# Kernel tuning notes

Hardware: AMD Instinct MI355X
Metric: run time of the kernel (lower is better)

## Reference

```python
import jax, jax.numpy as jnp
import numpy as np

B, N, S = 8, 8192, 2048
D1, D2 = 128, 256
IN_CH = D1 + D2  # 384
MLP = [256, 128]
BN_EPS = 1e-5


def setup_inputs() -> dict:
    key = jax.random.key(0)
    ks = jax.random.split(key, 12)
    inp = {
        'xyz1': jax.random.normal(ks[0], (B, 3, N), dtype=jnp.float32),
        'xyz2': jax.random.normal(ks[1], (B, 3, S), dtype=jnp.float32),
        'points1': jax.random.normal(ks[2], (B, D1, N), dtype=jnp.float32),
        'points2': jax.random.normal(ks[3], (B, D2, S), dtype=jnp.float32),
    }
    # Conv1d(kernel=1) weights [out, in] + bias, BN gamma/beta per layer
    c_in = IN_CH
    for i, c_out in enumerate(MLP):
        scale = 1.0 / np.sqrt(c_in)
        inp[f'w{i}'] = jax.random.uniform(ks[4 + 2 * i], (c_out, c_in), jnp.float32, -scale, scale)
        inp[f'b{i}'] = jax.random.uniform(ks[5 + 2 * i], (c_out,), jnp.float32, -scale, scale)
        inp[f'g{i}'] = jnp.ones((c_out,), jnp.float32)
        inp[f'be{i}'] = jnp.zeros((c_out,), jnp.float32)
        c_in = c_out
    return inp


def _fp_forward(xyz1, xyz2, points1, points2, params):
    # xyz1: [B,3,N] -> [B,N,3]; xyz2: [B,3,S] -> [B,S,3]
    p1 = jnp.transpose(xyz1, (0, 2, 1))
    p2 = jnp.transpose(xyz2, (0, 2, 1))
    # squared pairwise distances [B,N,S]
    dist = (jnp.sum(p1 * p1, -1)[:, :, None]
            + jnp.sum(p2 * p2, -1)[:, None, :]
            - 2.0 * jnp.einsum('bnc,bsc->bns', p1, p2))
    # 3 smallest distances per query point
    neg_d, idx = jax.lax.top_k(-dist, 3)          # idx: [B,N,3]
    d3 = -neg_d
    recip = 1.0 / (d3 + 1e-8)
    weight = recip / jnp.sum(recip, axis=2, keepdims=True)  # [B,N,3]
    # gather neighbor features: points2 [B,D2,S] -> [B,S,D2]
    feats = jnp.transpose(points2, (0, 2, 1))
    gathered = feats[jnp.arange(feats.shape[0])[:, None, None], idx]  # [B,N,3,D2]
    interp = jnp.einsum('bnkd,bnk->bdn', gathered, weight)            # [B,D2,N]
    x = jnp.concatenate([points1, interp], axis=1)                    # [B,D1+D2,N]
    # Conv1d(k=1) + BatchNorm1d(train-mode batch stats) + ReLU stack
    for w, b, g, be in params:
        x = jnp.einsum('oc,bcn->bon', w, x) + b[None, :, None]
        mean = jnp.mean(x, axis=(0, 2), keepdims=True)
        var = jnp.mean((x - mean) ** 2, axis=(0, 2), keepdims=True)
        x = (x - mean) * jax.lax.rsqrt(var + BN_EPS)
        x = x * g[None, :, None] + be[None, :, None]
        x = jax.nn.relu(x)
    return x


def reference(xyz1, xyz2, points1, points2, w0, b0, g0, be0, w1, b1, g1, be1):
    params = [(w0, b0, g0, be0), (w1, b1, g1, be1)]
    return _fp_forward(xyz1, xyz2, points1, points2, params)
```

## Files before the change

kernel.cpp:

```cpp
#include <hip/hip_runtime.h>

#define NB   8
#define NPT  8192
#define NS   2048
#define ND1  128
#define ND2  256
#define NIN  384
#define NC0  256
#define NC1  128
#define NBN  (NB*NPT)

typedef __bf16 bf16x8 __attribute__((ext_vector_type(8)));
typedef __bf16 bf16x4 __attribute__((ext_vector_type(4)));
typedef float  f32x4  __attribute__((ext_vector_type(4)));

#define SWZ(n, off) ((off) ^ (((n) & 7) << 4))

__global__ __launch_bounds__(256) void knn_kernel(
    const float* __restrict__ xyz1, const float* __restrict__ xyz2,
    int* __restrict__ idx3, float* __restrict__ wgt3)
{
    __shared__ float4 pts[NS];
    __shared__ float md[64][4][3];
    __shared__ int   mi[64][4][3];

    const int b  = blockIdx.x;
    const int qt = blockIdx.y;
    const float* x2 = xyz2 + (size_t)b * 3 * NS;
    for (int s = threadIdx.x; s < NS; s += 256) {
        float x = x2[s], y = x2[NS + s], z = x2[2 * NS + s];
        pts[s] = make_float4(x, y, z, x * x + y * y + z * z);
    }
    __syncthreads();

    const int q    = threadIdx.x & 63;
    const int part = threadIdx.x >> 6;
    const int n    = qt * 64 + q;
    const float* x1 = xyz1 + (size_t)b * 3 * NPT;
    const float px = x1[n], py = x1[NPT + n], pz = x1[2 * NPT + n];
    const float qx = -2.f * px, qy = -2.f * py, qz = -2.f * pz;

    float d0 = 3e38f, d1 = 3e38f, d2 = 3e38f;
    int   i0 = 0, i1 = 0, i2 = 0;
    const int sbeg = part * (NS / 4);
    #pragma unroll 2
    for (int s = sbeg; s < sbeg + NS / 4; ++s) {
        float4 p = pts[s];
        float d = fmaf(qx, p.x, fmaf(qy, p.y, fmaf(qz, p.z, p.w)));
        bool c0 = d < d0, c1 = d < d1, c2 = d < d2;
        i2 = c1 ? i1 : (c2 ? s : i2);
        i1 = c0 ? i0 : (c1 ? s : i1);
        i0 = c0 ? s  : i0;
        d2 = fminf(fmaxf(d, d1), d2);
        d1 = fminf(fmaxf(d, d0), d1);
        d0 = fminf(d, d0);
    }
    md[q][part][0] = d0; md[q][part][1] = d1; md[q][part][2] = d2;
    mi[q][part][0] = i0; mi[q][part][1] = i1; mi[q][part][2] = i2;
    __syncthreads();

    if (threadIdx.x < 64) {
        int hp[4] = {0, 0, 0, 0};
        float rd[3]; int ri[3];
        #pragma unroll
        for (int k = 0; k < 3; ++k) {
            float best = 3.0e38f; int bl = 0;
            #pragma unroll
            for (int l = 0; l < 4; ++l) {
                float dv = md[q][l][hp[l]];
                if (dv < best) { best = dv; bl = l; }
            }
            rd[k] = best; ri[k] = mi[q][bl][hp[bl]]; hp[bl]++;
        }
        const float p1sq = px * px + py * py + pz * pz;
        float r0 = 1.0f / (rd[0] + p1sq + 1e-8f);
        float r1 = 1.0f / (rd[1] + p1sq + 1e-8f);
        float r2 = 1.0f / (rd[2] + p1sq + 1e-8f);
        float inv = 1.0f / (r0 + r1 + r2);
        size_t base = ((size_t)b * NPT + n) * 3;
        idx3[base] = ri[0]; idx3[base + 1] = ri[1]; idx3[base + 2] = ri[2];
        wgt3[base] = r0 * inv; wgt3[base + 1] = r1 * inv; wgt3[base + 2] = r2 * inv;
    }
}

__global__ __launch_bounds__(256) void transpose_p2_kernel(
    const float* __restrict__ p2, __bf16* __restrict__ p2t)
{
    __shared__ float tile[64][65];
    const int b  = blockIdx.x;
    const int ts = (blockIdx.y & 31) * 64;
    const int td = (blockIdx.y >> 5) * 64;
    const int sl = threadIdx.x & 63, dl = threadIdx.x >> 6;
    #pragma unroll
    for (int i = 0; i < 16; ++i)
        tile[dl + 4 * i][sl] = p2[((size_t)b * ND2 + td + dl + 4 * i) * NS + ts + sl];
    __syncthreads();
    const int dl2 = threadIdx.x & 63, sl2 = threadIdx.x >> 6;
    #pragma unroll
    for (int i = 0; i < 16; ++i)
        p2t[((size_t)b * NS + ts + sl2 + 4 * i) * ND2 + td + dl2] =
            (__bf16)tile[dl2][sl2 + 4 * i];
}

__global__ __launch_bounds__(256) void transpose_p1_kernel(
    const float* __restrict__ p1, __bf16* __restrict__ XcP1)
{
    __shared__ float tile[64][65];
    const int b  = blockIdx.x;
    const int tn = (blockIdx.y & 127) * 64;
    const int tc = (blockIdx.y >> 7) * 64;
    const int sl = threadIdx.x & 63, dl = threadIdx.x >> 6;
    #pragma unroll
    for (int i = 0; i < 16; ++i)
        tile[dl + 4 * i][sl] = p1[((size_t)b * ND1 + tc + dl + 4 * i) * NPT + tn + sl];
    __syncthreads();
    const int n_local = threadIdx.x >> 2, c16 = threadIdx.x & 3;
    __bf16* dst = XcP1 + ((size_t)b * NPT + tn + n_local) * ND1 + tc + c16 * 16;
    bf16x8 v0, v1;
    #pragma unroll
    for (int k = 0; k < 8; ++k) {
        v0[k] = (__bf16)tile[c16 * 16 + k][n_local];
        v1[k] = (__bf16)tile[c16 * 16 + 8 + k][n_local];
    }
    *(bf16x8*)dst = v0;
    *(bf16x8*)(dst + 8) = v1;
}

__global__ __launch_bounds__(256) void convert_w_kernel(
    const float* __restrict__ w0, const float* __restrict__ w1,
    __bf16* __restrict__ Wb0, __bf16* __restrict__ Wb1)
{
    const int t = blockIdx.x * 256 + threadIdx.x;
    if (t < NC0 * NIN) Wb0[t] = (__bf16)w0[t];
    if (t < NC1 * NC0) Wb1[t] = (__bf16)w1[t];
}

__global__ __launch_bounds__(512, 4) void gemm0_fused(
    const __bf16* __restrict__ Wb, const __bf16* __restrict__ XcP1,
    const __bf16* __restrict__ p2t,
    const int* __restrict__ idx3, const float* __restrict__ wgt3,
    __bf16* __restrict__ y0, float* __restrict__ sums, float* __restrict__ sumsq)
{
    __shared__ char BsRaw[64 * NIN * 2];
    __shared__ float red[2][NC0][2];
    char* lds = BsRaw;

    const int tid = threadIdx.x;
    const int bn0 = blockIdx.x * 64;
    const int b   = bn0 / NPT;

    #pragma unroll
    for (int i = 0; i < 2; ++i) {
        const int id = tid + i * 512;
        const int n  = id >> 4;
        const int c8 = (id & 15) * 8;
        bf16x8 v = *(const bf16x8*)&XcP1[(size_t)(bn0 + n) * ND1 + c8];
        *(bf16x8*)(lds + n * (NIN * 2) + SWZ(n, c8 * 2)) = v;
    }

    {
        const int ng   = tid >> 3;
        const int part = tid & 7;
        const size_t base3 = (size_t)(bn0 + ng) * 3;
        const int i0 = idx3[base3], i1 = idx3[base3 + 1], i2 = idx3[base3 + 2];
        const float w0 = wgt3[base3], w1 = wgt3[base3 + 1], w2 = wgt3[base3 + 2];
        const __bf16* r0 = p2t + ((size_t)b * NS + i0) * ND2;
        const __bf16* r1 = p2t + ((size_t)b * NS + i1) * ND2;
        const __bf16* r2 = p2t + ((size_t)b * NS + i2) * ND2;
        #pragma unroll
        for (int i = 0; i < 4; ++i) {
            const int d0 = part * 32 + i * 8;
            bf16x8 a = *(const bf16x8*)(r0 + d0);
            bf16x8 c = *(const bf16x8*)(r1 + d0);
            bf16x8 e = *(const bf16x8*)(r2 + d0);
            bf16x8 v;
            #pragma unroll
            for (int j = 0; j < 8; ++j)
                v[j] = (__bf16)(w0 * (float)a[j] + w1 * (float)c[j] + w2 * (float)e[j]);
            *(bf16x8*)(lds + ng * (NIN * 2) + SWZ(ng, (ND1 + d0) * 2)) = v;
        }
    }
    __syncthreads();

    const int l = tid & 63, w = tid >> 6;
    const int g = l >> 4, lm = l & 15;
    const int ow = w >> 1, nw = w & 1;
    const int o_base = ow * 64;

    f32x4 acc[4][2] = {};

    for (int k0 = 0; k0 < NIN; k0 += 32) {
        const int kk = k0 + g * 8;
        bf16x8 af[4], bfr[2];
        #pragma unroll
        for (int m = 0; m < 4; ++m)
            af[m] = *(const bf16x8*)&Wb[(size_t)(o_base + m * 16 + lm) * NIN + kk];
        #pragma unroll
        for (int r = 0; r < 2; ++r) {
            const int n_lds = nw * 32 + r * 16 + lm;
            bfr[r] = *(const bf16x8*)(lds + n_lds * (NIN * 2) + SWZ(n_lds, kk * 2));
        }
        #pragma unroll
        for (int m = 0; m < 4; ++m)
            #pragma unroll
            for (int r = 0; r < 2; ++r)
                acc[m][r] = __builtin_amdgcn_mfma_f32_16x16x32_bf16(af[m], bfr[r], acc[m][r], 0, 0, 0);
    }

    #pragma unroll
    for (int m = 0; m < 4; ++m) {
        float s[4] = {0.f, 0.f, 0.f, 0.f}, q[4] = {0.f, 0.f, 0.f, 0.f};
        #pragma unroll
        for (int r = 0; r < 2; ++r) {
            const int n = nw * 32 + r * 16 + lm;
            bf16x4 pk;
            #pragma unroll
            for (int j = 0; j < 4; ++j) {
                float v = acc[m][r][j];
                pk[j] = (__bf16)v;
                s[j] += v; q[j] += v * v;
            }
            *(bf16x4*)&y0[(size_t)(bn0 + n) * NC0 + o_base + m * 16 + g * 4] = pk;
        }
        #pragma unroll
        for (int j = 0; j < 4; ++j) {
            #pragma unroll
            for (int st = 1; st < 16; st <<= 1) {
                s[j] += __shfl_xor(s[j], st);
                q[j] += __shfl_xor(q[j], st);
            }
        }
        if (lm == 0) {
            #pragma unroll
            for (int j = 0; j < 4; ++j) {
                red[0][o_base + m * 16 + g * 4 + j][nw] = s[j];
                red[1][o_base + m * 16 + g * 4 + j][nw] = q[j];
            }
        }
    }
    __syncthreads();
    if (tid < NC0) {
        atomicAdd(&sums[tid],  red[0][tid][0] + red[0][tid][1]);
        atomicAdd(&sumsq[tid], red[1][tid][0] + red[1][tid][1]);
    }
}

__global__ void stats_kernel(
    const float* __restrict__ sums, const float* __restrict__ sumsq,
    const float* __restrict__ g, const float* __restrict__ be,
    float* __restrict__ scale, float* __restrict__ shift, int C)
{
    int c = blockIdx.x * blockDim.x + threadIdx.x;
    if (c < C) {
        const float invN = 1.0f / (float)NBN;
        float mean = sums[c] * invN;
        float var  = sumsq[c] * invN - mean * mean;
        float sc   = g[c] * rsqrtf(var + 1e-5f);
        scale[c] = sc;
        shift[c] = be[c] - mean * sc;
    }
}

__global__ __launch_bounds__(512, 4) void gemm1_mfma(
    const __bf16* __restrict__ Wb, const __bf16* __restrict__ y0,
    const float* __restrict__ scale0, const float* __restrict__ shift0,
    __bf16* __restrict__ y1, float* __restrict__ sums, float* __restrict__ sumsq)
{
    __shared__ float red[2][NC1][4];
    const int tid = threadIdx.x;
    const int l = tid & 63, w = tid >> 6;
    const int g = l >> 4, lm = l & 15;
    const int ow = w >> 2, nw = w & 3;
    const int o_base = ow * 64;
    const int n_base = blockIdx.x * 128 + nw * 32;

    f32x4 acc[4][2] = {};

    for (int k0 = 0; k0 < NC0; k0 += 32) {
        const int kk = k0 + g * 8;
        f32x4 sc0 = *(const f32x4*)&scale0[kk];
        f32x4 sc1 = *(const f32x4*)&scale0[kk + 4];
        f32x4 sh0 = *(const f32x4*)&shift0[kk];
        f32x4 sh1 = *(const f32x4*)&shift0[kk + 4];
        bf16x8 af[4], bfr[2];
        #pragma unroll
        for (int m = 0; m < 4; ++m)
            af[m] = *(const bf16x8*)&Wb[(size_t)(o_base + m * 16 + lm) * NC0 + kk];
        #pragma unroll
        for (int r = 0; r < 2; ++r) {
            bf16x8 raw = *(const bf16x8*)&y0[(size_t)(n_base + r * 16 + lm) * NC0 + kk];
            bf16x8 bb;
            #pragma unroll
            for (int j = 0; j < 4; ++j) {
                bb[j]     = (__bf16)fmaxf((float)raw[j]     * sc0[j] + sh0[j], 0.f);
                bb[j + 4] = (__bf16)fmaxf((float)raw[j + 4] * sc1[j] + sh1[j], 0.f);
            }
            bfr[r] = bb;
        }
        #pragma unroll
        for (int m = 0; m < 4; ++m)
            #pragma unroll
            for (int r = 0; r < 2; ++r)
                acc[m][r] = __builtin_amdgcn_mfma_f32_16x16x32_bf16(af[m], bfr[r], acc[m][r], 0, 0, 0);
    }

    #pragma unroll
    for (int m = 0; m < 4; ++m) {
        float s[4] = {0.f, 0.f, 0.f, 0.f}, q[4] = {0.f, 0.f, 0.f, 0.f};
        #pragma unroll
        for (int r = 0; r < 2; ++r) {
            const int n = n_base + r * 16 + lm;
            #pragma unroll
            for (int j = 0; j < 4; ++j) {
                float v = acc[m][r][j];
                y1[(size_t)(o_base + m * 16 + g * 4 + j) * NBN + n] = (__bf16)v;
                s[j] += v; q[j] += v * v;
            }
        }
        #pragma unroll
        for (int j = 0; j < 4; ++j) {
            #pragma unroll
            for (int st = 1; st < 16; st <<= 1) {
                s[j] += __shfl_xor(s[j], st);
                q[j] += __shfl_xor(q[j], st);
            }
        }
        if (lm == 0) {
            #pragma unroll
            for (int j = 0; j < 4; ++j) {
                red[0][o_base + m * 16 + g * 4 + j][nw] = s[j];
                red[1][o_base + m * 16 + g * 4 + j][nw] = q[j];
            }
        }
    }
    __syncthreads();
    if (tid < NC1) {
        atomicAdd(&sums[tid],  red[0][tid][0] + red[0][tid][1] + red[0][tid][2] + red[0][tid][3]);
        atomicAdd(&sumsq[tid], red[1][tid][0] + red[1][tid][1] + red[1][tid][2] + red[1][tid][3]);
    }
}

__global__ __launch_bounds__(256) void bnout_kernel(
    const __bf16* __restrict__ y1, const float* __restrict__ scale1,
    const float* __restrict__ shift1, float* __restrict__ out)
{
    const size_t t = (size_t)blockIdx.x * 256 + threadIdx.x;
    const size_t e = t * 8;
    const int n = (int)(e & (NPT - 1));
    const int o = (int)((e >> 13) & (NC1 - 1));
    const int b = (int)(e >> 20);
    bf16x8 v = *(const bf16x8*)&y1[(size_t)o * NBN + (size_t)b * NPT + n];
    const float s = scale1[o], sh = shift1[o];
    f32x4 r0, r1;
    #pragma unroll
    for (int j = 0; j < 4; ++j) {
        r0[j] = fmaxf((float)v[j]     * s + sh, 0.f);
        r1[j] = fmaxf((float)v[j + 4] * s + sh, 0.f);
    }
    *(f32x4*)&out[e]     = r0;
    *(f32x4*)&out[e + 4] = r1;
}

extern "C" void kernel_launch(void* const* d_in, const int* in_sizes, int n_in,
                              void* d_out, int out_size, void* d_ws, size_t ws_size,
                              hipStream_t stream)
{
    const float* xyz1    = (const float*)d_in[0];
    const float* xyz2    = (const float*)d_in[1];
    const float* points1 = (const float*)d_in[2];
    const float* points2 = (const float*)d_in[3];
    const float* w0  = (const float*)d_in[4];
    const float* g0  = (const float*)d_in[6];
    const float* be0 = (const float*)d_in[7];
    const float* w1  = (const float*)d_in[8];
    const float* g1  = (const float*)d_in[10];
    const float* be1 = (const float*)d_in[11];

    char* ws = (char*)d_ws;
    size_t off = 0;
    int*    idx3 = (int*)(ws + off);    off += (size_t)NBN * 3 * 4;
    float*  wgt3 = (float*)(ws + off);  off += (size_t)NBN * 3 * 4;
    __bf16* XcP1 = (__bf16*)(ws + off); off += (size_t)NBN * ND1 * 2;
    __bf16* y0   = (__bf16*)(ws + off); off += (size_t)NBN * NC0 * 2;
    __bf16* y1   = (__bf16*)(ws + off); off += (size_t)NC1 * NBN * 2;
    __bf16* p2t  = (__bf16*)(ws + off); off += (size_t)NB * NS * ND2 * 2;
    __bf16* Wb0  = (__bf16*)(ws + off); off += (size_t)NC0 * NIN * 2;
    __bf16* Wb1  = (__bf16*)(ws + off); off += (size_t)NC1 * NC0 * 2;
    float*  stats = (float*)(ws + off);
    float* sums0  = stats;        float* sumsq0 = stats + 256;
    float* sums1  = stats + 512;  float* sumsq1 = stats + 640;
    float* scale0 = stats + 768;  float* shift0 = stats + 1024;
    float* scale1 = stats + 1280; float* shift1 = stats + 1408;

    hipMemsetAsync(stats, 0, 768 * 4, stream);

    convert_w_kernel   <<<dim3(NC0 * NIN / 256), 256, 0, stream>>>(w0, w1, Wb0, Wb1);
    transpose_p2_kernel<<<dim3(NB, 128), 256, 0, stream>>>(points2, p2t);
    transpose_p1_kernel<<<dim3(NB, 256), 256, 0, stream>>>(points1, XcP1);
    knn_kernel         <<<dim3(NB, 128), 256, 0, stream>>>(xyz1, xyz2, idx3, wgt3);
    gemm0_fused        <<<dim3(NBN / 64), 512, 0, stream>>>(
        Wb0, XcP1, p2t, idx3, wgt3, y0, sums0, sumsq0);
    stats_kernel       <<<1, 256, 0, stream>>>(sums0, sumsq0, g0, be0, scale0, shift0, NC0);
    gemm1_mfma         <<<dim3(NBN / 128), 512, 0, stream>>>(Wb1, y0, scale0, shift0, y1, sums1, sumsq1);
    stats_kernel       <<<1, 128, 0, stream>>>(sums1, sumsq1, g1, be1, scale1, shift1, NC1);
    bnout_kernel       <<<dim3(NBN * NC1 / 8 / 256), 256, 0, stream>>>(y1, scale1, shift1, (float*)d_out);
}
```

Baseline: 328.9 us.

## Overlap neighbor gather with points1 GEMM phase and shrink LDS tile

The fused GEMM0 kernel no longer stages the points1 slice in LDS. It reads those B fragments straight from global memory for the first 128 K-steps. The interpolated-neighbor gather is split into two halves whose global loads are issued before MFMA work, so gather latency overlaps the points1 GEMM. LDS shrinks from 64x384 to 64x256 bf16, which may raise occupancy, but points1 fragments now come from uncoalesced global loads.

```diff
diff --git a/kernel.cpp b/kernel.cpp
--- a/kernel.cpp
+++ b/kernel.cpp
@@ -141,46 +141,21 @@
     const int* __restrict__ idx3, const float* __restrict__ wgt3,
     __bf16* __restrict__ y0, float* __restrict__ sums, float* __restrict__ sumsq)
 {
-    __shared__ char BsRaw[64 * NIN * 2];
+    __shared__ char Bs[64 * ND2 * 2];
     __shared__ float red[2][NC0][2];
-    char* lds = BsRaw;
 
     const int tid = threadIdx.x;
     const int bn0 = blockIdx.x * 64;
     const int b   = bn0 / NPT;
 
-    #pragma unroll
-    for (int i = 0; i < 2; ++i) {
-        const int id = tid + i * 512;
-        const int n  = id >> 4;
-        const int c8 = (id & 15) * 8;
-        bf16x8 v = *(const bf16x8*)&XcP1[(size_t)(bn0 + n) * ND1 + c8];
-        *(bf16x8*)(lds + n * (NIN * 2) + SWZ(n, c8 * 2)) = v;
-    }
-
-    {
-        const int ng   = tid >> 3;
-        const int part = tid & 7;
-        const size_t base3 = (size_t)(bn0 + ng) * 3;
-        const int i0 = idx3[base3], i1 = idx3[base3 + 1], i2 = idx3[base3 + 2];
-        const float w0 = wgt3[base3], w1 = wgt3[base3 + 1], w2 = wgt3[base3 + 2];
-        const __bf16* r0 = p2t + ((size_t)b * NS + i0) * ND2;
-        const __bf16* r1 = p2t + ((size_t)b * NS + i1) * ND2;
-        const __bf16* r2 = p2t + ((size_t)b * NS + i2) * ND2;
-        #pragma unroll
-        for (int i = 0; i < 4; ++i) {
-            const int d0 = part * 32 + i * 8;
-            bf16x8 a = *(const bf16x8*)(r0 + d0);
-            bf16x8 c = *(const bf16x8*)(r1 + d0);
-            bf16x8 e = *(const bf16x8*)(r2 + d0);
-            bf16x8 v;
-            #pragma unroll
-            for (int j = 0; j < 8; ++j)
-                v[j] = (__bf16)(w0 * (float)a[j] + w1 * (float)c[j] + w2 * (float)e[j]);
-            *(bf16x8*)(lds + ng * (NIN * 2) + SWZ(ng, (ND1 + d0) * 2)) = v;
-        }
-    }
-    __syncthreads();
+    const int ng   = tid >> 3;
+    const int part = tid & 7;
+    const size_t base3 = (size_t)(bn0 + ng) * 3;
+    const int gi0 = idx3[base3], gi1 = idx3[base3 + 1], gi2 = idx3[base3 + 2];
+    const float gw0 = wgt3[base3], gw1 = wgt3[base3 + 1], gw2 = wgt3[base3 + 2];
+    const __bf16* r0 = p2t + ((size_t)b * NS + gi0) * ND2;
+    const __bf16* r1 = p2t + ((size_t)b * NS + gi1) * ND2;
+    const __bf16* r2 = p2t + ((size_t)b * NS + gi2) * ND2;
 
     const int l = tid & 63, w = tid >> 6;
     const int g = l >> 4, lm = l & 15;
@@ -189,7 +164,17 @@
 
     f32x4 acc[4][2] = {};
 
-    for (int k0 = 0; k0 < NIN; k0 += 32) {
+    bf16x8 rawA0, rawA1, rawA2, rawB0, rawB1, rawB2;
+    {
+        const int d0 = part * 32;
+        rawA0 = *(const bf16x8*)(r0 + d0);     rawA1 = *(const bf16x8*)(r1 + d0);
+        rawA2 = *(const bf16x8*)(r2 + d0);
+        rawB0 = *(const bf16x8*)(r0 + d0 + 8); rawB1 = *(const bf16x8*)(r1 + d0 + 8);
+        rawB2 = *(const bf16x8*)(r2 + d0 + 8);
+    }
+
+    #pragma unroll
+    for (int k0 = 0; k0 < 64; k0 += 32) {
         const int kk = k0 + g * 8;
         bf16x8 af[4], bfr[2];
         #pragma unroll
@@ -197,8 +182,78 @@
             af[m] = *(const bf16x8*)&Wb[(size_t)(o_base + m * 16 + lm) * NIN + kk];
         #pragma unroll
         for (int r = 0; r < 2; ++r) {
+            const int n = nw * 32 + r * 16 + lm;
+            bfr[r] = *(const bf16x8*)&XcP1[(size_t)(bn0 + n) * ND1 + kk];
+        }
+        #pragma unroll
+        for (int m = 0; m < 4; ++m)
+            #pragma unroll
+            for (int r = 0; r < 2; ++r)
+                acc[m][r] = __builtin_amdgcn_mfma_f32_16x16x32_bf16(af[m], bfr[r], acc[m][r], 0, 0, 0);
+    }
+
+    {
+        bf16x8 v0, v1;
+        #pragma unroll
+        for (int j = 0; j < 8; ++j) {
+            v0[j] = (__bf16)(gw0 * (float)rawA0[j] + gw1 * (float)rawA1[j] + gw2 * (float)rawA2[j]);
+            v1[j] = (__bf16)(gw0 * (float)rawB0[j] + gw1 * (float)rawB1[j] + gw2 * (float)rawB2[j]);
+        }
+        const int d0 = part * 32;
+        *(bf16x8*)(Bs + ng * (ND2 * 2) + SWZ(ng, d0 * 2))       = v0;
+        *(bf16x8*)(Bs + ng * (ND2 * 2) + SWZ(ng, (d0 + 8) * 2)) = v1;
+    }
+    {
+        const int d0 = part * 32 + 16;
+        rawA0 = *(const bf16x8*)(r0 + d0);     rawA1 = *(const bf16x8*)(r1 + d0);
+        rawA2 = *(const bf16x8*)(r2 + d0);
+        rawB0 = *(const bf16x8*)(r0 + d0 + 8); rawB1 = *(const bf16x8*)(r1 + d0 + 8);
+        rawB2 = *(const bf16x8*)(r2 + d0 + 8);
+    }
+
+    #pragma unroll
+    for (int k0 = 64; k0 < 128; k0 += 32) {
+        const int kk = k0 + g * 8;
+        bf16x8 af[4], bfr[2];
+        #pragma unroll
+        for (int m = 0; m < 4; ++m)
+            af[m] = *(const bf16x8*)&Wb[(size_t)(o_base + m * 16 + lm) * NIN + kk];
+        #pragma unroll
+        for (int r = 0; r < 2; ++r) {
+            const int n = nw * 32 + r * 16 + lm;
+            bfr[r] = *(const bf16x8*)&XcP1[(size_t)(bn0 + n) * ND1 + kk];
+        }
+        #pragma unroll
+        for (int m = 0; m < 4; ++m)
+            #pragma unroll
+            for (int r = 0; r < 2; ++r)
+                acc[m][r] = __builtin_amdgcn_mfma_f32_16x16x32_bf16(af[m], bfr[r], acc[m][r], 0, 0, 0);
+    }
+
+    {
+        bf16x8 v0, v1;
+        #pragma unroll
+        for (int j = 0; j < 8; ++j) {
+            v0[j] = (__bf16)(gw0 * (float)rawA0[j] + gw1 * (float)rawA1[j] + gw2 * (float)rawA2[j]);
+            v1[j] = (__bf16)(gw0 * (float)rawB0[j] + gw1 * (float)rawB1[j] + gw2 * (float)rawB2[j]);
+        }
+        const int d0 = part * 32 + 16;
+        *(bf16x8*)(Bs + ng * (ND2 * 2) + SWZ(ng, d0 * 2))       = v0;
+        *(bf16x8*)(Bs + ng * (ND2 * 2) + SWZ(ng, (d0 + 8) * 2)) = v1;
+    }
+    __syncthreads();
+
+    #pragma unroll
+    for (int k0 = 128; k0 < NIN; k0 += 32) {
+        const int kd = k0 - 128 + g * 8;
+        bf16x8 af[4], bfr[2];
+        #pragma unroll
+        for (int m = 0; m < 4; ++m)
+            af[m] = *(const bf16x8*)&Wb[(size_t)(o_base + m * 16 + lm) * NIN + k0 + g * 8];
+        #pragma unroll
+        for (int r = 0; r < 2; ++r) {
             const int n_lds = nw * 32 + r * 16 + lm;
-            bfr[r] = *(const bf16x8*)(lds + n_lds * (NIN * 2) + SWZ(n_lds, kk * 2));
+            bfr[r] = *(const bf16x8*)(Bs + n_lds * (ND2 * 2) + SWZ(n_lds, kd * 2));
         }
         #pragma unroll
         for (int m = 0; m < 4; ++m)
```

After: 327.9 us. Within noise of the previous version (-0.3%).
